# Kernel optimization log

Measured on AMD Instinct MI355X. Metric: run time of the kernel, lower is better.

The kernel has to match this reference:

```python
import jax, jax.numpy as jnp
import numpy as np
from functools import reduce

N_QUBITS = 4
N_LAYERS = 3
DIM = 2 ** N_QUBITS  # 16

I2 = jnp.eye(2, dtype=jnp.complex64)

def _cnot_mat(c, t, n=N_QUBITS):
    # big-endian (PennyLane) ordering: wire 0 is the most significant bit
    M = np.zeros((2 ** n, 2 ** n), dtype=np.complex64)
    for idx in range(2 ** n):
        if (idx >> (n - 1 - c)) & 1:
            new = idx ^ (1 << (n - 1 - t))
        else:
            new = idx
        M[new, idx] = 1.0
    return jnp.asarray(M)

# entangling layer: CNOT(0,1), CNOT(1,2), CNOT(2,3), CNOT(3,0)
_ENT = reduce(lambda A, B: B @ A,
              [_cnot_mat(i, i + 1) for i in range(N_QUBITS - 1)] + [_cnot_mat(N_QUBITS - 1, 0)],
              jnp.eye(DIM, dtype=jnp.complex64))

# PauliZ expectation sign table: zs[idx, i] = +1/-1 for bit i of basis state idx
_ZS = jnp.asarray(
    np.array([[1.0 - 2.0 * ((idx >> (N_QUBITS - 1 - i)) & 1) for i in range(N_QUBITS)]
              for idx in range(DIM)], dtype=np.float32))

def _ry(t):
    c, s = jnp.cos(t / 2), jnp.sin(t / 2)
    return jnp.stack([jnp.stack([c, -s]), jnp.stack([s, c])]).astype(jnp.complex64)

def _rz(t):
    e = jnp.exp(-0.5j * t.astype(jnp.complex64))
    return jnp.stack([jnp.stack([e, 0.0 * e]), jnp.stack([0.0 * e, jnp.conj(e)])])

def _embed(g, w):
    mats = [I2] * w + [g] + [I2] * (N_QUBITS - 1 - w)
    return reduce(jnp.kron, mats)

def _variational_unitary(params):
    # fixed (data-independent) 16x16 unitary for the whole variational circuit
    U = jnp.eye(DIM, dtype=jnp.complex64)
    off = 0
    for _ in range(N_LAYERS):
        for i in range(N_QUBITS):
            U = _embed(_ry(params[off]), i) @ U; off += 1
            U = _embed(_rz(params[off]), i) @ U; off += 1
            U = _embed(_ry(params[off]), i) @ U; off += 1
        U = _ENT @ U
    return U

def setup_inputs() -> dict:
    key = jax.random.key(0)
    k1, k2 = jax.random.split(key)
    x = jax.random.uniform(k1, (4096, 784), dtype=jnp.float32)
    params = jax.random.normal(k2, (36,), dtype=jnp.float32)
    return {"x": x, "params": params}

def reference(x, params):
    bsz = x.shape[0]
    # 2x2 non-overlapping patches, row-major over (r, c): [bsz, 196, 4]
    img = x.reshape(bsz, 14, 2, 14, 2)
    patches = img.transpose(0, 1, 3, 2, 4).reshape(bsz, 196, 4)
    theta = (patches * jnp.pi).reshape(bsz * 196, 4)  # RY encoding angles
    # RY(theta)|0> = [cos(theta/2), sin(theta/2)] -> product state over 4 qubits
    a, b = jnp.cos(theta / 2), jnp.sin(theta / 2)
    q = jnp.stack([a, b], axis=-1).astype(jnp.complex64)  # [N, 4, 2]
    psi0 = jnp.einsum('na,nb,nc,nd->nabcd', q[:, 0], q[:, 1], q[:, 2], q[:, 3]).reshape(-1, DIM)
    U = _variational_unitary(params)
    psi = psi0 @ U.T  # [N, 16]
    probs = (psi.real ** 2 + psi.imag ** 2).astype(jnp.float32)
    expvals = probs @ _ZS  # [N, 4] Pauli-Z expectations
    return expvals.reshape(bsz, 196 * 4)
```

## Files before the change

### kernel.cpp

```cpp
#include <hip/hip_runtime.h>
#include <math.h>

#define DIM 16

typedef __attribute__((ext_vector_type(8))) _Float16 half8;
typedef __attribute__((ext_vector_type(16))) float f32x16;

__global__ __launch_bounds__(64) void build_unitary_kernel(
    const float* __restrict__ params, float* __restrict__ Amat) {
  __shared__ float s_c[36], s_s[36];
  const int t = threadIdx.x;
  if (t < 36) {
    const float half = params[t] * 0.5f;
    s_c[t] = cosf(half);
    s_s[t] = sinf(half);
  }
  __syncthreads();
  if (t >= DIM) return;
  const int col = t;

  float vr[DIM], vi[DIM];
#pragma unroll
  for (int k = 0; k < DIM; ++k) { vr[k] = (k == col) ? 1.0f : 0.0f; vi[k] = 0.0f; }

  int off = 0;
#pragma unroll
  for (int layer = 0; layer < 3; ++layer) {
#pragma unroll
    for (int w = 0; w < 4; ++w) {
      const int m = 1 << (3 - w);
      {
        const float cy = s_c[off], sy = s_s[off]; ++off;
#pragma unroll
        for (int k0 = 0; k0 < DIM; ++k0) {
          if (k0 & m) continue;
          const int k1 = k0 | m;
          const float ar = vr[k0], ai = vi[k0], br = vr[k1], bi = vi[k1];
          vr[k0] = cy * ar - sy * br;  vi[k0] = cy * ai - sy * bi;
          vr[k1] = sy * ar + cy * br;  vi[k1] = sy * ai + cy * bi;
        }
      }
      {
        const float cz = s_c[off], sz = s_s[off]; ++off;
#pragma unroll
        for (int k = 0; k < DIM; ++k) {
          const float sg = (k & m) ? sz : -sz;
          const float ar = vr[k], ai = vi[k];
          vr[k] = cz * ar - sg * ai;
          vi[k] = cz * ai + sg * ar;
        }
      }
      {
        const float cy = s_c[off], sy = s_s[off]; ++off;
#pragma unroll
        for (int k0 = 0; k0 < DIM; ++k0) {
          if (k0 & m) continue;
          const int k1 = k0 | m;
          const float ar = vr[k0], ai = vi[k0], br = vr[k1], bi = vi[k1];
          vr[k0] = cy * ar - sy * br;  vi[k0] = cy * ai - sy * bi;
          vr[k1] = sy * ar + cy * br;  vi[k1] = sy * ai + cy * bi;
        }
      }
    }
#pragma unroll
    for (int g = 0; g < 4; ++g) {
      const int a = (g < 3) ? g : 3;
      const int b = (g < 3) ? (g + 1) : 0;
      const int ca = 1 << (3 - a);
      const int tb = 1 << (3 - b);
#pragma unroll
      for (int r = 0; r < DIM; ++r) {
        if ((r & ca) && !(r & tb)) {
          const int r2 = r | tb;
          float tmp;
          tmp = vr[r]; vr[r] = vr[r2]; vr[r2] = tmp;
          tmp = vi[r]; vi[r] = vi[r2]; vi[r2] = tmp;
        }
      }
    }
  }
#pragma unroll
  for (int n = 0; n < DIM; ++n) {
    Amat[n * 16 + col]        = vr[n];
    Amat[(16 + n) * 16 + col] = vi[n];
  }
}

__global__ __launch_bounds__(256) void quanv_mfma_kernel(
    const float* __restrict__ x, const float* __restrict__ Amat,
    float* __restrict__ out, int npatch) {
  const int tid  = threadIdx.x;
  const int lane = tid & 63;
  const int wave = tid >> 6;
  const int nl   = lane & 31;
  const int h    = lane >> 5;

  const float4* Arow = (const float4*)(Amat + nl * 16 + 8 * h);
  const float4 ua = Arow[0];
  const float4 ub = Arow[1];
  const float uf[8] = {ua.x, ua.y, ua.z, ua.w, ub.x, ub.y, ub.z, ub.w};
  half8 Uh, Ul;
#pragma unroll
  for (int j = 0; j < 8; ++j) {
    const _Float16 vh = (_Float16)uf[j];
    Uh[j] = vh;
    Ul[j] = (_Float16)(uf[j] - (float)vh);
  }

  const int base = blockIdx.x * 256 + wave * 64;

#pragma unroll
  for (int it = 0; it < 2; ++it) {
    int n = base + it * 32 + nl;
    if (n >= npatch) n = npatch - 1;
    const unsigned nu = (unsigned)n;
    const unsigned b  = nu / 196u;
    const unsigned p  = nu - b * 196u;
    const unsigned r1 = p / 14u;
    const unsigned c1 = p - r1 * 14u;
    const float* xb = x + b * 784u + r1 * 56u + c1 * 2u;
    const float2 t0 = *(const float2*)(xb);
    const float2 t1 = *(const float2*)(xb + 28);

    const float HPI = 1.57079632679489662f;
    float c0, s0, c1q, s1q, c2q, s2q, c3q, s3q;
    __sincosf(t0.x * HPI, &s0,  &c0);
    __sincosf(t0.y * HPI, &s1q, &c1q);
    __sincosf(t1.x * HPI, &s2q, &c2q);
    __sincosf(t1.y * HPI, &s3q, &c3q);

    const float f   = h ? s0 : c0;
    const float ab0 = f * c1q, ab1 = f * s1q;
    const float cd[4] = {c2q * c3q, c2q * s3q, s2q * c3q, s2q * s3q};
    half8 bfrag;
#pragma unroll
    for (int j = 0; j < 8; ++j)
      bfrag[j] = (_Float16)(((j & 4) ? ab1 : ab0) * cd[j & 3]);

    f32x16 C;
#pragma unroll
    for (int r = 0; r < 16; ++r) C[r] = 0.0f;
    C = __builtin_amdgcn_mfma_f32_32x32x16_f16(Uh, bfrag, C, 0, 0, 0);
    C = __builtin_amdgcn_mfma_f32_32x32x16_f16(Ul, bfrag, C, 0, 0, 0);

    float pq[8];
#pragma unroll
    for (int r = 0; r < 8; ++r) pq[r] = fmaf(C[r], C[r], C[r + 8] * C[r + 8]);

    const float s03 = pq[0] + pq[3], s12 = pq[1] + pq[2];
    const float s47 = pq[4] + pq[7], s56 = pq[5] + pq[6];
    float e0 = (s03 + s12) - (s47 + s56);
    float e1 = (s03 + s12) + (s47 + s56);  e1 = h ? -e1 : e1;
    float e2 = ((pq[0] + pq[1]) - (pq[2] + pq[3]))
             + ((pq[4] + pq[5]) - (pq[6] + pq[7]));
    float e3 = ((pq[0] - pq[1]) + (pq[2] - pq[3]))
             + ((pq[4] - pq[5]) + (pq[6] - pq[7]));
    e0 += __shfl_xor(e0, 32, 64);
    e1 += __shfl_xor(e1, 32, 64);
    e2 += __shfl_xor(e2, 32, 64);
    e3 += __shfl_xor(e3, 32, 64);

    if (h == 0 && n < npatch)
      ((float4*)out)[n] = make_float4(e0, e1, e2, e3);
  }
}

extern "C" void kernel_launch(void* const* d_in, const int* in_sizes, int n_in,
                              void* d_out, int out_size, void* d_ws, size_t ws_size,
                              hipStream_t stream) {
  const float* x      = (const float*)d_in[0];
  const float* params = (const float*)d_in[1];
  float* out  = (float*)d_out;
  float* Amat = (float*)d_ws;

  build_unitary_kernel<<<1, 64, 0, stream>>>(params, Amat);

  const int npatch = in_sizes[0] / 4;
  const int nblk = (npatch + 255) / 256;
  quanv_mfma_kernel<<<nblk, 256, 0, stream>>>(x, Amat, out, npatch);
}
```

Measured before the change: 76.54 us.

## Fuse unitary construction into the MFMA kernel and double patches per block

Removes the separate single-block kernel that built the 16x16 unitary. Each block of the main kernel now recomputes the unitary redundantly into shared memory, which drops a kernel launch and the serial dependency between the two kernels. To spread that per-block setup over more work, each block now handles 512 patches (4 iterations per wave) instead of 256. The cost is 16 threads per block running a long serial gate simulation while the rest wait at a barrier, plus fewer blocks in flight.

```diff
diff --git a/kernel.cpp b/kernel.cpp
--- a/kernel.cpp
+++ b/kernel.cpp
@@ -6,96 +6,96 @@
 typedef __attribute__((ext_vector_type(8))) _Float16 half8;
 typedef __attribute__((ext_vector_type(16))) float f32x16;
 
-__global__ __launch_bounds__(64) void build_unitary_kernel(
-    const float* __restrict__ params, float* __restrict__ Amat) {
+__global__ __launch_bounds__(256) void quanv_fused_kernel(
+    const float* __restrict__ x, const float* __restrict__ params,
+    float* __restrict__ out, int npatch) {
   __shared__ float s_c[36], s_s[36];
-  const int t = threadIdx.x;
-  if (t < 36) {
-    const float half = params[t] * 0.5f;
-    s_c[t] = cosf(half);
-    s_s[t] = sinf(half);
-  }
-  __syncthreads();
-  if (t >= DIM) return;
-  const int col = t;
+  __shared__ __align__(16) float sA[512];
 
-  float vr[DIM], vi[DIM];
-#pragma unroll
-  for (int k = 0; k < DIM; ++k) { vr[k] = (k == col) ? 1.0f : 0.0f; vi[k] = 0.0f; }
-
-  int off = 0;
-#pragma unroll
-  for (int layer = 0; layer < 3; ++layer) {
-#pragma unroll
-    for (int w = 0; w < 4; ++w) {
-      const int m = 1 << (3 - w);
-      {
-        const float cy = s_c[off], sy = s_s[off]; ++off;
-#pragma unroll
-        for (int k0 = 0; k0 < DIM; ++k0) {
-          if (k0 & m) continue;
-          const int k1 = k0 | m;
-          const float ar = vr[k0], ai = vi[k0], br = vr[k1], bi = vi[k1];
-          vr[k0] = cy * ar - sy * br;  vi[k0] = cy * ai - sy * bi;
-          vr[k1] = sy * ar + cy * br;  vi[k1] = sy * ai + cy * bi;
-        }
-      }
-      {
-        const float cz = s_c[off], sz = s_s[off]; ++off;
-#pragma unroll
-        for (int k = 0; k < DIM; ++k) {
-          const float sg = (k & m) ? sz : -sz;
-          const float ar = vr[k], ai = vi[k];
-          vr[k] = cz * ar - sg * ai;
-          vi[k] = cz * ai + sg * ar;
-        }
-      }
-      {
-        const float cy = s_c[off], sy = s_s[off]; ++off;
-#pragma unroll
-        for (int k0 = 0; k0 < DIM; ++k0) {
-          if (k0 & m) continue;
-          const int k1 = k0 | m;
-          const float ar = vr[k0], ai = vi[k0], br = vr[k1], bi = vi[k1];
-          vr[k0] = cy * ar - sy * br;  vi[k0] = cy * ai - sy * bi;
-          vr[k1] = sy * ar + cy * br;  vi[k1] = sy * ai + cy * bi;
-        }
-      }
-    }
-#pragma unroll
-    for (int g = 0; g < 4; ++g) {
-      const int a = (g < 3) ? g : 3;
-      const int b = (g < 3) ? (g + 1) : 0;
-      const int ca = 1 << (3 - a);
-      const int tb = 1 << (3 - b);
-#pragma unroll
-      for (int r = 0; r < DIM; ++r) {
-        if ((r & ca) && !(r & tb)) {
-          const int r2 = r | tb;
-          float tmp;
-          tmp = vr[r]; vr[r] = vr[r2]; vr[r2] = tmp;
-          tmp = vi[r]; vi[r] = vi[r2]; vi[r2] = tmp;
-        }
-      }
-    }
-  }
-#pragma unroll
-  for (int n = 0; n < DIM; ++n) {
-    Amat[n * 16 + col]        = vr[n];
-    Amat[(16 + n) * 16 + col] = vi[n];
-  }
-}
-
-__global__ __launch_bounds__(256) void quanv_mfma_kernel(
-    const float* __restrict__ x, const float* __restrict__ Amat,
-    float* __restrict__ out, int npatch) {
   const int tid  = threadIdx.x;
   const int lane = tid & 63;
   const int wave = tid >> 6;
   const int nl   = lane & 31;
   const int h    = lane >> 5;
 
-  const float4* Arow = (const float4*)(Amat + nl * 16 + 8 * h);
+  if (tid < 36) {
+    float s, c;
+    __sincosf(params[tid] * 0.5f, &s, &c);
+    s_c[tid] = c; s_s[tid] = s;
+  }
+  __syncthreads();
+
+  if (tid < DIM) {
+    const int col = tid;
+    float vr[DIM], vi[DIM];
+#pragma unroll
+    for (int k = 0; k < DIM; ++k) { vr[k] = (k == col) ? 1.0f : 0.0f; vi[k] = 0.0f; }
+
+    int off = 0;
+#pragma unroll
+    for (int layer = 0; layer < 3; ++layer) {
+#pragma unroll
+      for (int w = 0; w < 4; ++w) {
+        const int m = 1 << (3 - w);
+        {
+          const float cy = s_c[off], sy = s_s[off]; ++off;
+#pragma unroll
+          for (int k0 = 0; k0 < DIM; ++k0) {
+            if (k0 & m) continue;
+            const int k1 = k0 | m;
+            const float ar = vr[k0], ai = vi[k0], br = vr[k1], bi = vi[k1];
+            vr[k0] = cy * ar - sy * br;  vi[k0] = cy * ai - sy * bi;
+            vr[k1] = sy * ar + cy * br;  vi[k1] = sy * ai + cy * bi;
+          }
+        }
+        {
+          const float cz = s_c[off], sz = s_s[off]; ++off;
+#pragma unroll
+          for (int k = 0; k < DIM; ++k) {
+            const float sg = (k & m) ? sz : -sz;
+            const float ar = vr[k], ai = vi[k];
+            vr[k] = cz * ar - sg * ai;
+            vi[k] = cz * ai + sg * ar;
+          }
+        }
+        {
+          const float cy = s_c[off], sy = s_s[off]; ++off;
+#pragma unroll
+          for (int k0 = 0; k0 < DIM; ++k0) {
+            if (k0 & m) continue;
+            const int k1 = k0 | m;
+            const float ar = vr[k0], ai = vi[k0], br = vr[k1], bi = vi[k1];
+            vr[k0] = cy * ar - sy * br;  vi[k0] = cy * ai - sy * bi;
+            vr[k1] = sy * ar + cy * br;  vi[k1] = sy * ai + cy * bi;
+          }
+        }
+      }
+#pragma unroll
+      for (int g = 0; g < 4; ++g) {
+        const int a = (g < 3) ? g : 3;
+        const int b = (g < 3) ? (g + 1) : 0;
+        const int ca = 1 << (3 - a);
+        const int tb = 1 << (3 - b);
+#pragma unroll
+        for (int r = 0; r < DIM; ++r) {
+          if ((r & ca) && !(r & tb)) {
+            const int r2 = r | tb;
+            float tmp;
+            tmp = vr[r]; vr[r] = vr[r2]; vr[r2] = tmp;
+            tmp = vi[r]; vi[r] = vi[r2]; vi[r2] = tmp;
+          }
+        }
+      }
+    }
+#pragma unroll
+    for (int n = 0; n < DIM; ++n) {
+      sA[n * 16 + col]        = vr[n];
+      sA[(16 + n) * 16 + col] = vi[n];
+    }
+  }
+  __syncthreads();
+
+  const float4* Arow = (const float4*)(sA + nl * 16 + 8 * h);
   const float4 ua = Arow[0];
   const float4 ub = Arow[1];
   const float uf[8] = {ua.x, ua.y, ua.z, ua.w, ub.x, ub.y, ub.z, ub.w};
@@ -107,10 +107,10 @@
     Ul[j] = (_Float16)(uf[j] - (float)vh);
   }
 
-  const int base = blockIdx.x * 256 + wave * 64;
+  const int base = blockIdx.x * 512 + wave * 128;
 
 #pragma unroll
-  for (int it = 0; it < 2; ++it) {
+  for (int it = 0; it < 4; ++it) {
     int n = base + it * 32 + nl;
     if (n >= npatch) n = npatch - 1;
     const unsigned nu = (unsigned)n;
@@ -170,12 +170,10 @@
                               hipStream_t stream) {
   const float* x      = (const float*)d_in[0];
   const float* params = (const float*)d_in[1];
-  float* out  = (float*)d_out;
-  float* Amat = (float*)d_ws;
-
-  build_unitary_kernel<<<1, 64, 0, stream>>>(params, Amat);
+  float* out = (float*)d_out;
+  (void)d_ws; (void)ws_size;
 
   const int npatch = in_sizes[0] / 4;
-  const int nblk = (npatch + 255) / 256;
-  quanv_mfma_kernel<<<nblk, 256, 0, stream>>>(x, Amat, out, npatch);
+  const int nblk = (npatch + 511) / 512;
+  quanv_fused_kernel<<<nblk, 256, 0, stream>>>(x, params, out, npatch);
 }
```

Result: no change. 76.98 us (+0.6%).
